# Kernel optimization log

Hardware: AMD Instinct MI355X
Metric: run time of the kernel (lower is better)

Reference implementation:

```python
import jax, jax.numpy as jnp
import numpy as np

N_NEURONS, RANK, N_CONV, LY, LX, BATCH = 8192, 1, 64, 36, 36, 256


def setup_inputs() -> dict:
    key = jax.random.key(0)
    k1, k2, k3, k4 = jax.random.split(key, 4)
    conv = jax.random.normal(k1, (BATCH, N_CONV, LY, LX), dtype=jnp.float32)
    Wc = 0.01 * jax.random.normal(k2, (N_NEURONS, RANK, N_CONV), dtype=jnp.float32)
    Wy = 0.01 * jax.random.normal(k3, (N_NEURONS, RANK, LY), dtype=jnp.float32)
    Wx = 0.01 * jax.random.normal(k4, (N_NEURONS, RANK, LX), dtype=jnp.float32)
    bias = jnp.zeros((N_NEURONS,), dtype=jnp.float32)
    return {"conv": conv, "Wc": Wc, "Wy": Wy, "Wx": Wx, "bias": bias}


def reference(conv, Wc, Wy, Wx, bias):
    # yx_separable, rank == 1 path of Readout.forward:
    #   pred = einsum('nrc,nry,icyx,nrx->in', Wc, Wy, conv, Wx)
    #   pred = elu(pred + bias)
    # Staged contraction: build per-neuron rank-1 spatial filter, contract
    # spatial dims first (small y*x=1296), then channels.
    Wyx = jnp.einsum('nry,nrx->nryx', Wy, Wx)              # [N, R, Ly, Lx]
    s = jnp.einsum('icyx,nryx->inrc', conv, Wyx)           # [B, N, R, C]
    pred = jnp.einsum('inrc,nrc->in', s, Wc)               # [B, N]
    return jax.nn.elu(pred + bias)
```

## Files before the change

### kernel.cpp

```cpp
#include <hip/hip_runtime.h>
#include <hip/hip_bf16.h>

#define NNEUR 8192
#define NCONV 64
#define LYC   36
#define LXC   36
#define BATCH 256
#define KRAW  1296
#define KPAD  1344
#define KITER 21
#define MROWS 16384
#define BM 256
#define BN 128
#define BK 64
#define ACH_PER_IT 2048
#define BCH_PER_IT 1024
#define A_TILE_H   (KITER * ACH_PER_IT * 8)
#define B_TILE_H   (KITER * BCH_PER_IT * 8)

typedef __attribute__((ext_vector_type(8))) _Float16 half8;
typedef __attribute__((ext_vector_type(4))) float f32x4;
typedef __attribute__((ext_vector_type(16))) float f32x16;

__device__ __forceinline__ void async_copy16(const void* g, void* l) {
  __builtin_amdgcn_global_load_lds(
      (const __attribute__((address_space(1))) void*)g,
      (__attribute__((address_space(3))) void*)l, 16, 0, 0);
}

__global__ __launch_bounds__(256) void prep_kernel(
    const float* __restrict__ conv, const float* __restrict__ Wy,
    const float* __restrict__ Wx, _Float16* __restrict__ A,
    _Float16* __restrict__ B) {
  const int t = threadIdx.x;
  const int bx = blockIdx.x;
  const int tile = blockIdx.y;
  const int c = t & 7;
  half8 h;
  if (bx < 168) {
    const int it = bx >> 3, i = bx & 7;
    const int r = (t >> 3) + 32 * i;
    const int k0 = it * 64 + c * 8;
    const int grow = tile * BM + r;
    if (k0 < KRAW) {
      const float* s = conv + (size_t)grow * KRAW + k0;
#pragma unroll
      for (int e = 0; e < 8; e++) h[e] = (_Float16)s[e];
    } else {
#pragma unroll
      for (int e = 0; e < 8; e++) h[e] = (_Float16)0.f;
    }
    *(half8*)(A + (size_t)tile * A_TILE_H + (size_t)it * (ACH_PER_IT * 8) +
              ((size_t)c * 256 + r) * 8) = h;
  } else {
    const int bxp = bx - 168;
    const int it = bxp >> 2, i4 = bxp & 3;
    const int r = (t >> 3) + 32 * i4;
    const int k0 = it * 64 + c * 8;
    const int n = tile * BN + r;
    if (k0 < KRAW) {
      const float* wyn = Wy + n * LYC;
      const float* wxn = Wx + n * LXC;
      int y = k0 / LXC;
      int x = k0 - y * LXC;
#pragma unroll
      for (int e = 0; e < 8; e++) {
        h[e] = (_Float16)(wyn[y] * wxn[x] * 256.f);
        if (++x == LXC) { x = 0; ++y; }
      }
    } else {
#pragma unroll
      for (int e = 0; e < 8; e++) h[e] = (_Float16)0.f;
    }
    *(half8*)(B + (size_t)tile * B_TILE_H + (size_t)it * (BCH_PER_IT * 8) +
              ((size_t)c * 128 + r) * 8) = h;
  }
}

__global__ __launch_bounds__(256, 3) void gemm_fused_kernel(
    const _Float16* __restrict__ A, const _Float16* __restrict__ B,
    const float* __restrict__ Wc, const float* __restrict__ bias,
    float* __restrict__ out) {
  __shared__ _Float16 As[BM * BK];
  __shared__ _Float16 Bs[BN * BK];

  const int bid = blockIdx.x;
  const int l = bid >> 3;
  const int ntile = (bid & 7) * 8 + (l & 7);
  const int mtile = l >> 3;
  const int tileN = ntile * BN;

  const int t = threadIdx.x;
  const int lane = t & 63;
  const int wave = t >> 6;
  const int wm = wave >> 1, wn = wave & 1;
  const int r32 = lane & 31, hh = lane >> 5;

  f32x16 acc[4][2] = {};

  const _Float16* pA = A + (size_t)mtile * A_TILE_H;
  const _Float16* pB = B + (size_t)ntile * B_TILE_H;
  _Float16* lA = As + t * 8;
  _Float16* lB = Bs + t * 8;

  for (int it = 0; it < KITER; it++) {
    const _Float16* sA = pA + (size_t)it * (ACH_PER_IT * 8) + t * 8;
    const _Float16* sB = pB + (size_t)it * (BCH_PER_IT * 8) + t * 8;
#pragma unroll
    for (int i = 0; i < 8; i++) async_copy16(sA + i * 2048, lA + i * 2048);
#pragma unroll
    for (int i = 0; i < 4; i++) async_copy16(sB + i * 2048, lB + i * 2048);
    __syncthreads();

#pragma unroll
    for (int ks = 0; ks < 4; ks++) {
      const int cc = 2 * ks + hh;
      half8 bf[2];
#pragma unroll
      for (int nb = 0; nb < 2; nb++) {
        const int r = wn * 64 + nb * 32 + r32;
        bf[nb] = *(const half8*)(Bs + cc * 1024 + r * 8);
      }
#pragma unroll
      for (int mb = 0; mb < 4; mb++) {
        const int r = wm * 128 + mb * 32 + r32;
        const half8 af = *(const half8*)(As + cc * 2048 + r * 8);
#pragma unroll
        for (int nb = 0; nb < 2; nb++)
          acc[mb][nb] = __builtin_amdgcn_mfma_f32_32x32x16_f16(
              af, bf[nb], acc[mb][nb], 0, 0, 0);
      }
    }
    __syncthreads();
  }

  const int ibase = mtile * 4 + wm * 2;
  float v[2][2];
#pragma unroll
  for (int nb = 0; nb < 2; nb++) {
    const int n_g = tileN + wn * 64 + nb * 32 + r32;
    const float* wc = Wc + (size_t)n_g * NCONV;
    f32x4 w[2][4];
#pragma unroll
    for (int hf = 0; hf < 2; hf++)
#pragma unroll
      for (int g = 0; g < 4; g++)
        w[hf][g] = *(const f32x4*)(wc + hf * 32 + hh * 4 + g * 8);
#pragma unroll
    for (int img = 0; img < 2; img++) {
      float p = 0.f;
#pragma unroll
      for (int hf = 0; hf < 2; hf++)
#pragma unroll
        for (int g = 0; g < 4; g++)
#pragma unroll
          for (int q = 0; q < 4; q++)
            p += acc[img * 2 + hf][nb][g * 4 + q] * w[hf][g][q];
      p += __shfl_xor(p, 32);
      v[img][nb] = p;
    }
  }
  const int img = ibase + hh;
#pragma unroll
  for (int nb = 0; nb < 2; nb++) {
    const int n_out = tileN + wn * 64 + nb * 32 + r32;
    float z = v[hh][nb] * 0.00390625f + bias[n_out];
    z = z > 0.f ? z : (__expf(z) - 1.f);
    out[(size_t)img * NNEUR + n_out] = z;
  }
}

extern "C" void kernel_launch(void* const* d_in, const int* in_sizes, int n_in,
                              void* d_out, int out_size, void* d_ws,
                              size_t ws_size, hipStream_t stream) {
  const float* conv = (const float*)d_in[0];
  const float* Wc = (const float*)d_in[1];
  const float* Wy = (const float*)d_in[2];
  const float* Wx = (const float*)d_in[3];
  const float* bias = (const float*)d_in[4];
  float* out = (float*)d_out;

  _Float16* Abuf = (_Float16*)d_ws;
  _Float16* Bbuf = (_Float16*)((char*)d_ws + (size_t)MROWS * KPAD * 2);

  prep_kernel<<<dim3(252, 64), 256, 0, stream>>>(conv, Wy, Wx, Abuf, Bbuf);
  gemm_fused_kernel<<<4096, 256, 0, stream>>>(Abuf, Bbuf, Wc, bias, out);
}
```

Measured before the change: 485.6 us.

## Halve M tile and double-buffer LDS with async prefetch of next K slice

Result: slower. 555.2 us (+14.3%).

```diff
diff --git a/kernel.cpp b/kernel.cpp
--- a/kernel.cpp
+++ b/kernel.cpp
@@ -10,13 +10,11 @@
 #define KPAD  1344
 #define KITER 21
 #define MROWS 16384
-#define BM 256
+#define BM 128
 #define BN 128
 #define BK 64
-#define ACH_PER_IT 2048
-#define BCH_PER_IT 1024
-#define A_TILE_H   (KITER * ACH_PER_IT * 8)
-#define B_TILE_H   (KITER * BCH_PER_IT * 8)
+#define IT_H     8192
+#define TILE_H   (KITER * IT_H)
 
 typedef __attribute__((ext_vector_type(8))) _Float16 half8;
 typedef __attribute__((ext_vector_type(4))) float f32x4;
@@ -34,11 +32,11 @@
     _Float16* __restrict__ B) {
   const int t = threadIdx.x;
   const int bx = blockIdx.x;
-  const int tile = blockIdx.y;
   const int c = t & 7;
   half8 h;
-  if (bx < 168) {
-    const int it = bx >> 3, i = bx & 7;
+  if (bx < 84) {
+    const int tile = blockIdx.y;
+    const int it = bx >> 2, i = bx & 3;
     const int r = (t >> 3) + 32 * i;
     const int k0 = it * 64 + c * 8;
     const int grow = tile * BM + r;
@@ -50,12 +48,14 @@
 #pragma unroll
       for (int e = 0; e < 8; e++) h[e] = (_Float16)0.f;
     }
-    *(half8*)(A + (size_t)tile * A_TILE_H + (size_t)it * (ACH_PER_IT * 8) +
-              ((size_t)c * 256 + r) * 8) = h;
+    *(half8*)(A + (size_t)tile * TILE_H + (size_t)it * IT_H +
+              ((size_t)c * 128 + r) * 8) = h;
   } else {
-    const int bxp = bx - 168;
-    const int it = bxp >> 2, i4 = bxp & 3;
-    const int r = (t >> 3) + 32 * i4;
+    const int tile = blockIdx.y;
+    if (tile >= 64) return;
+    const int bxp = bx - 84;
+    const int it = bxp >> 2, i = bxp & 3;
+    const int r = (t >> 3) + 32 * i;
     const int k0 = it * 64 + c * 8;
     const int n = tile * BN + r;
     if (k0 < KRAW) {
@@ -72,17 +72,17 @@
 #pragma unroll
       for (int e = 0; e < 8; e++) h[e] = (_Float16)0.f;
     }
-    *(half8*)(B + (size_t)tile * B_TILE_H + (size_t)it * (BCH_PER_IT * 8) +
+    *(half8*)(B + (size_t)tile * TILE_H + (size_t)it * IT_H +
               ((size_t)c * 128 + r) * 8) = h;
   }
 }
 
-__global__ __launch_bounds__(256, 3) void gemm_fused_kernel(
+__global__ __launch_bounds__(256, 2) void gemm_fused_kernel(
     const _Float16* __restrict__ A, const _Float16* __restrict__ B,
     const float* __restrict__ Wc, const float* __restrict__ bias,
     float* __restrict__ out) {
-  __shared__ _Float16 As[BM * BK];
-  __shared__ _Float16 Bs[BN * BK];
+  __shared__ _Float16 As[2][BM * BK];
+  __shared__ _Float16 Bs[2][BN * BK];
 
   const int bid = blockIdx.x;
   const int l = bid >> 3;
@@ -96,77 +96,78 @@
   const int wm = wave >> 1, wn = wave & 1;
   const int r32 = lane & 31, hh = lane >> 5;
 
-  f32x16 acc[4][2] = {};
+  f32x16 acc[2][2] = {};
 
-  const _Float16* pA = A + (size_t)mtile * A_TILE_H;
-  const _Float16* pB = B + (size_t)ntile * B_TILE_H;
-  _Float16* lA = As + t * 8;
-  _Float16* lB = Bs + t * 8;
+  const _Float16* pA = A + (size_t)mtile * TILE_H + t * 8;
+  const _Float16* pB = B + (size_t)ntile * TILE_H + t * 8;
 
-  for (int it = 0; it < KITER; it++) {
-    const _Float16* sA = pA + (size_t)it * (ACH_PER_IT * 8) + t * 8;
-    const _Float16* sB = pB + (size_t)it * (BCH_PER_IT * 8) + t * 8;
+  auto stage = [&](int b, int it) {
+    const _Float16* sA = pA + (size_t)it * IT_H;
+    const _Float16* sB = pB + (size_t)it * IT_H;
+    _Float16* lA = &As[b][t * 8];
+    _Float16* lB = &Bs[b][t * 8];
 #pragma unroll
-    for (int i = 0; i < 8; i++) async_copy16(sA + i * 2048, lA + i * 2048);
+    for (int i = 0; i < 4; i++) async_copy16(sA + i * 2048, lA + i * 2048);
 #pragma unroll
     for (int i = 0; i < 4; i++) async_copy16(sB + i * 2048, lB + i * 2048);
-    __syncthreads();
+  };
 
+  stage(0, 0);
+#pragma unroll 1
+  for (int it = 0; it < KITER; ++it) {
+    const int cbuf = it & 1;
+    if (it + 1 < KITER) {
+      stage(cbuf ^ 1, it + 1);
+      asm volatile("s_waitcnt vmcnt(8)" ::: "memory");
+    } else {
+      asm volatile("s_waitcnt vmcnt(0)" ::: "memory");
+    }
+    __builtin_amdgcn_s_barrier();
 #pragma unroll
     for (int ks = 0; ks < 4; ks++) {
       const int cc = 2 * ks + hh;
-      half8 bf[2];
+      half8 bf[2], af[2];
 #pragma unroll
       for (int nb = 0; nb < 2; nb++) {
         const int r = wn * 64 + nb * 32 + r32;
-        bf[nb] = *(const half8*)(Bs + cc * 1024 + r * 8);
+        bf[nb] = *(const half8*)(&Bs[cbuf][cc * 1024 + r * 8]);
       }
 #pragma unroll
-      for (int mb = 0; mb < 4; mb++) {
-        const int r = wm * 128 + mb * 32 + r32;
-        const half8 af = *(const half8*)(As + cc * 2048 + r * 8);
+      for (int mb = 0; mb < 2; mb++) {
+        const int r = wm * 64 + mb * 32 + r32;
+        af[mb] = *(const half8*)(&As[cbuf][cc * 1024 + r * 8]);
+      }
+#pragma unroll
+      for (int mb = 0; mb < 2; mb++)
 #pragma unroll
         for (int nb = 0; nb < 2; nb++)
           acc[mb][nb] = __builtin_amdgcn_mfma_f32_32x32x16_f16(
-              af, bf[nb], acc[mb][nb], 0, 0, 0);
-      }
+              af[mb], bf[nb], acc[mb][nb], 0, 0, 0);
     }
-    __syncthreads();
+    __builtin_amdgcn_s_barrier();
   }
 
-  const int ibase = mtile * 4 + wm * 2;
-  float v[2][2];
+  const int img = mtile * 2 + wm;
 #pragma unroll
   for (int nb = 0; nb < 2; nb++) {
     const int n_g = tileN + wn * 64 + nb * 32 + r32;
     const float* wc = Wc + (size_t)n_g * NCONV;
-    f32x4 w[2][4];
+    float p = 0.f;
 #pragma unroll
-    for (int hf = 0; hf < 2; hf++)
+    for (int mb = 0; mb < 2; mb++)
 #pragma unroll
-      for (int g = 0; g < 4; g++)
-        w[hf][g] = *(const f32x4*)(wc + hf * 32 + hh * 4 + g * 8);
+      for (int g = 0; g < 4; g++) {
+        const f32x4 w = *(const f32x4*)(wc + mb * 32 + hh * 4 + g * 8);
 #pragma unroll
-    for (int img = 0; img < 2; img++) {
-      float p = 0.f;
-#pragma unroll
-      for (int hf = 0; hf < 2; hf++)
-#pragma unroll
-        for (int g = 0; g < 4; g++)
-#pragma unroll
-          for (int q = 0; q < 4; q++)
-            p += acc[img * 2 + hf][nb][g * 4 + q] * w[hf][g][q];
-      p += __shfl_xor(p, 32);
-      v[img][nb] = p;
+        for (int q = 0; q < 4; q++)
+          p += acc[mb][nb][g * 4 + q] * w[q];
+      }
+    p += __shfl_xor(p, 32);
+    if (hh == 0) {
+      float z = p * 0.00390625f + bias[n_g];
+      z = z > 0.f ? z : (__expf(z) - 1.f);
+      out[(size_t)img * NNEUR + n_g] = z;
     }
-  }
-  const int img = ibase + hh;
-#pragma unroll
-  for (int nb = 0; nb < 2; nb++) {
-    const int n_out = tileN + wn * 64 + nb * 32 + r32;
-    float z = v[hh][nb] * 0.00390625f + bias[n_out];
-    z = z > 0.f ? z : (__expf(z) - 1.f);
-    out[(size_t)img * NNEUR + n_out] = z;
   }
 }
 
@@ -183,6 +184,6 @@
   _Float16* Abuf = (_Float16*)d_ws;
   _Float16* Bbuf = (_Float16*)((char*)d_ws + (size_t)MROWS * KPAD * 2);
 
-  prep_kernel<<<dim3(252, 64), 256, 0, stream>>>(conv, Wy, Wx, Abuf, Bbuf);
-  gemm_fused_kernel<<<4096, 256, 0, stream>>>(Abuf, Bbuf, Wc, bias, out);
+  prep_kernel<<<dim3(168, 128), 256, 0, stream>>>(conv, Wy, Wx, Abuf, Bbuf);
+  gemm_fused_kernel<<<8192, 256, 0, stream>>>(Abuf, Bbuf, Wc, bias, out);
 }
```

## Restructure prep into per-k-iteration blocks with LDS transpose and rotated fp16 layout

Applied to the files above, without the earlier changes.

Measured after the change: 491.4 us. Within noise of the previous version (+1.2%).

```diff
diff --git a/kernel.cpp b/kernel.cpp
--- a/kernel.cpp
+++ b/kernel.cpp
@@ -32,33 +32,52 @@
     const float* __restrict__ conv, const float* __restrict__ Wy,
     const float* __restrict__ Wx, _Float16* __restrict__ A,
     _Float16* __restrict__ B) {
+  __shared__ _Float16 lds[2048 * 8];
+  half8* slots = (half8*)lds;
   const int t = threadIdx.x;
-  const int bx = blockIdx.x;
+  const int it = blockIdx.x;
   const int tile = blockIdx.y;
   const int c = t & 7;
-  half8 h;
-  if (bx < 168) {
-    const int it = bx >> 3, i = bx & 7;
-    const int r = (t >> 3) + 32 * i;
-    const int k0 = it * 64 + c * 8;
-    const int grow = tile * BM + r;
-    if (k0 < KRAW) {
-      const float* s = conv + (size_t)grow * KRAW + k0;
-#pragma unroll
-      for (int e = 0; e < 8; e++) h[e] = (_Float16)s[e];
+  const int rb = t >> 3;
+  const int k0 = it * 64 + c * 8;
+  const bool kv = (k0 < KRAW);
+
+  const float* convb = conv + (size_t)tile * BM * KRAW;
+#pragma unroll
+  for (int j = 0; j < 8; ++j) {
+    const int r = rb + 32 * j;
+    half8 h;
+    if (kv) {
+      const f32x4* sp = (const f32x4*)(convb + (size_t)r * KRAW + k0);
+      const f32x4 lo = sp[0], hi = sp[1];
+#pragma unroll
+      for (int e = 0; e < 4; e++) {
+        h[e] = (_Float16)lo[e];
+        h[e + 4] = (_Float16)hi[e];
+      }
     } else {
 #pragma unroll
       for (int e = 0; e < 8; e++) h[e] = (_Float16)0.f;
     }
-    *(half8*)(A + (size_t)tile * A_TILE_H + (size_t)it * (ACH_PER_IT * 8) +
-              ((size_t)c * 256 + r) * 8) = h;
-  } else {
-    const int bxp = bx - 168;
-    const int it = bxp >> 2, i4 = bxp & 3;
-    const int r = (t >> 3) + 32 * i4;
-    const int k0 = it * 64 + c * 8;
+    slots[r * 8 + (c ^ (r & 7))] = h;
+  }
+  __syncthreads();
+  _Float16* Ab = A + (size_t)tile * A_TILE_H + (size_t)it * (ACH_PER_IT * 8);
+#pragma unroll
+  for (int j = 0; j < 8; ++j) {
+    const int q = t + 256 * j;
+    const int r = q >> 3, s = q & 7;
+    const int cq = (s - r) & 7;
+    *(half8*)(Ab + (size_t)q * 8) = slots[r * 8 + (cq ^ (r & 7))];
+  }
+  __syncthreads();
+
+#pragma unroll
+  for (int j = 0; j < 4; ++j) {
+    const int r = rb + 32 * j;
     const int n = tile * BN + r;
-    if (k0 < KRAW) {
+    half8 h;
+    if (kv) {
       const float* wyn = Wy + n * LYC;
       const float* wxn = Wx + n * LXC;
       int y = k0 / LXC;
@@ -72,8 +91,16 @@
 #pragma unroll
       for (int e = 0; e < 8; e++) h[e] = (_Float16)0.f;
     }
-    *(half8*)(B + (size_t)tile * B_TILE_H + (size_t)it * (BCH_PER_IT * 8) +
-              ((size_t)c * 128 + r) * 8) = h;
+    slots[r * 8 + (c ^ (r & 7))] = h;
+  }
+  __syncthreads();
+  _Float16* Bb = B + (size_t)tile * B_TILE_H + (size_t)it * (BCH_PER_IT * 8);
+#pragma unroll
+  for (int j = 0; j < 4; ++j) {
+    const int q = t + 256 * j;
+    const int r = q >> 3, s = q & 7;
+    const int cq = (s - r) & 7;
+    *(half8*)(Bb + (size_t)q * 8) = slots[r * 8 + (cq ^ (r & 7))];
   }
 }
 
@@ -119,12 +146,12 @@
 #pragma unroll
       for (int nb = 0; nb < 2; nb++) {
         const int r = wn * 64 + nb * 32 + r32;
-        bf[nb] = *(const half8*)(Bs + cc * 1024 + r * 8);
+        bf[nb] = *(const half8*)(Bs + r * 64 + ((cc + r) & 7) * 8);
       }
 #pragma unroll
       for (int mb = 0; mb < 4; mb++) {
         const int r = wm * 128 + mb * 32 + r32;
-        const half8 af = *(const half8*)(As + cc * 2048 + r * 8);
+        const half8 af = *(const half8*)(As + r * 64 + ((cc + r) & 7) * 8);
 #pragma unroll
         for (int nb = 0; nb < 2; nb++)
           acc[mb][nb] = __builtin_amdgcn_mfma_f32_32x32x16_f16(
@@ -183,6 +210,6 @@
   _Float16* Abuf = (_Float16*)d_ws;
   _Float16* Bbuf = (_Float16*)((char*)d_ws + (size_t)MROWS * KPAD * 2);
 
-  prep_kernel<<<dim3(252, 64), 256, 0, stream>>>(conv, Wy, Wx, Abuf, Bbuf);
+  prep_kernel<<<dim3(KITER, 64), 256, 0, stream>>>(conv, Wy, Wx, Abuf, Bbuf);
   gemm_fused_kernel<<<4096, 256, 0, stream>>>(Abuf, Bbuf, Wc, bias, out);
 }
```

## Double-buffer A tiles in LDS and load B fragments directly into registers

Applied to the files above, without the earlier changes.

New measurement: 509.1 us. 4.8% more time.

```diff
diff --git a/kernel.cpp b/kernel.cpp
--- a/kernel.cpp
+++ b/kernel.cpp
@@ -77,12 +77,11 @@
   }
 }
 
-__global__ __launch_bounds__(256, 3) void gemm_fused_kernel(
+__global__ __launch_bounds__(256, 2) void gemm_fused_kernel(
     const _Float16* __restrict__ A, const _Float16* __restrict__ B,
     const float* __restrict__ Wc, const float* __restrict__ bias,
     float* __restrict__ out) {
-  __shared__ _Float16 As[BM * BK];
-  __shared__ _Float16 Bs[BN * BK];
+  __shared__ _Float16 As[2][BM * BK];
 
   const int bid = blockIdx.x;
   const int l = bid >> 3;
@@ -100,38 +99,62 @@
 
   const _Float16* pA = A + (size_t)mtile * A_TILE_H;
   const _Float16* pB = B + (size_t)ntile * B_TILE_H;
-  _Float16* lA = As + t * 8;
-  _Float16* lB = Bs + t * 8;
-
-  for (int it = 0; it < KITER; it++) {
+
+  auto stage = [&](int b, int it) {
     const _Float16* sA = pA + (size_t)it * (ACH_PER_IT * 8) + t * 8;
-    const _Float16* sB = pB + (size_t)it * (BCH_PER_IT * 8) + t * 8;
+    _Float16* lA = &As[b][t * 8];
 #pragma unroll
     for (int i = 0; i < 8; i++) async_copy16(sA + i * 2048, lA + i * 2048);
-#pragma unroll
-    for (int i = 0; i < 4; i++) async_copy16(sB + i * 2048, lB + i * 2048);
-    __syncthreads();
-
+  };
+
+  half8 bq[8];
+  auto loadB = [&](int it) {
+    const _Float16* base = pB + (size_t)it * (BCH_PER_IT * 8);
+#pragma unroll
+    for (int ks = 0; ks < 4; ks++)
+#pragma unroll
+      for (int nb = 0; nb < 2; nb++) {
+        const int r = wn * 64 + nb * 32 + r32;
+        bq[ks * 2 + nb] =
+            *(const half8*)(base + ((size_t)(2 * ks + hh) * 128 + r) * 8);
+      }
+  };
+
+  stage(0, 0);
+  asm volatile("" ::: "memory");
+  loadB(0);
+
+#pragma unroll 1
+  for (int it = 0; it < KITER; ++it) {
+    const int cbuf = it & 1;
+    if (it + 1 < KITER) {
+      stage(cbuf ^ 1, it + 1);
+      asm volatile("s_waitcnt vmcnt(16)" ::: "memory");
+    } else {
+      asm volatile("s_waitcnt vmcnt(8)" ::: "memory");
+    }
+    __builtin_amdgcn_s_barrier();
 #pragma unroll
     for (int ks = 0; ks < 4; ks++) {
       const int cc = 2 * ks + hh;
-      half8 bf[2];
-#pragma unroll
-      for (int nb = 0; nb < 2; nb++) {
-        const int r = wn * 64 + nb * 32 + r32;
-        bf[nb] = *(const half8*)(Bs + cc * 1024 + r * 8);
-      }
+      half8 af[4];
 #pragma unroll
       for (int mb = 0; mb < 4; mb++) {
         const int r = wm * 128 + mb * 32 + r32;
-        const half8 af = *(const half8*)(As + cc * 2048 + r * 8);
+        af[mb] = *(const half8*)(&As[cbuf][cc * 2048 + r * 8]);
+      }
+#pragma unroll
+      for (int mb = 0; mb < 4; mb++)
 #pragma unroll
         for (int nb = 0; nb < 2; nb++)
           acc[mb][nb] = __builtin_amdgcn_mfma_f32_32x32x16_f16(
-              af, bf[nb], acc[mb][nb], 0, 0, 0);
-      }
-    }
-    __syncthreads();
+              af[mb], bq[ks * 2 + nb], acc[mb][nb], 0, 0, 0);
+    }
+    if (it + 1 < KITER) {
+      asm volatile("" ::: "memory");
+      loadB(it + 1);
+    }
+    __builtin_amdgcn_s_barrier();
   }
 
   const int ibase = mtile * 4 + wm * 2;
```
